# Kernel tuning notes

Measured on AMD Instinct MI355X. Metric: run time of the kernel, lower is better.

## Reference

```python
import jax, jax.numpy as jnp
import numpy as np

N = 20000      # total residues (nodes)
E = 320000     # contact edges
G = 16         # graphs in batch
D_IN = 1280    # ESM embedding dim
H = 256        # hidden channels (1=2=3)
C = 500        # GO classes
EPS = 1e-5


def setup_inputs() -> dict:
    key = jax.random.key(0)
    ks = jax.random.split(key, 16)
    s = 0.02
    return {
        "x": jax.random.normal(ks[0], (N, D_IN), jnp.float32),
        "edge_index": jax.random.randint(ks[1], (2, E), 0, N, jnp.int32),
        "edge_attr": jax.random.uniform(ks[2], (E, 1), jnp.float32),
        "batch": jnp.sort(jax.random.randint(ks[3], (N,), 0, G, jnp.int32)),
        "seq_emb": jax.random.normal(ks[4], (G, D_IN), jnp.float32),
        "W1": jax.random.normal(ks[5], (D_IN, H), jnp.float32) * s,
        "b1": jnp.zeros((H,), jnp.float32),
        "g1": jnp.ones((H,), jnp.float32),
        "be1": jnp.zeros((H,), jnp.float32),
        "W2": jax.random.normal(ks[6], (H, H), jnp.float32) * s,
        "b2": jnp.zeros((H,), jnp.float32),
        "g2": jnp.ones((H,), jnp.float32),
        "be2": jnp.zeros((H,), jnp.float32),
        "W3": jax.random.normal(ks[7], (H, H), jnp.float32) * s,
        "b3": jnp.zeros((H,), jnp.float32),
        "g3": jnp.ones((H,), jnp.float32),
        "be3": jnp.zeros((H,), jnp.float32),
        "fc1_w": jax.random.normal(ks[8], (D_IN, H), jnp.float32) * s,
        "fc1_b": jnp.zeros((H,), jnp.float32),
        "lin_w": jax.random.normal(ks[9], (H, C), jnp.float32) * s,
        "lin_b": jnp.zeros((C,), jnp.float32),
    }


def gcn_conv(x, row, col, ew, W, b):
    # PyG GCNConv: x' = D^{-1/2} (A + I) D^{-1/2} X W + b, with edge weights,
    # self-loops of weight 1, aggregation at target (col).
    xw = x @ W                                             # [N, H]
    deg = jax.ops.segment_sum(ew, col, num_segments=N) + 1.0
    dinv = jax.lax.rsqrt(deg)                              # [N]
    norm = dinv[row] * ew * dinv[col]                      # [E]
    agg = jax.ops.segment_sum(norm[:, None] * xw[row], col, num_segments=N)
    agg = agg + (dinv * dinv)[:, None] * xw                # self-loop term
    return agg + b


def batch_norm(x, g, b):
    # training-mode BN over the node dimension (biased variance, as torch)
    m = jnp.mean(x, axis=0)
    v = jnp.var(x, axis=0)
    return (x - m) * jax.lax.rsqrt(v + EPS) * g + b


def reference(x, edge_index, edge_attr, batch, seq_emb,
              W1, b1, g1, be1, W2, b2, g2, be2, W3, b3, g3, be3,
              fc1_w, fc1_b, lin_w, lin_b):
    row, col = edge_index[0], edge_index[1]
    ew = edge_attr[:, 0]

    h = batch_norm(jax.nn.relu(gcn_conv(x, row, col, ew, W1, b1)), g1, be1)
    h = batch_norm(jax.nn.relu(gcn_conv(h, row, col, ew, W2, b2)), g2, be2)
    h = batch_norm(gcn_conv(h, row, col, ew, W3, b3), g3, be3)

    # global_mean_pool over graphs
    sums = jax.ops.segment_sum(h, batch, num_segments=G)        # [G, H]
    cnt = jax.ops.segment_sum(jnp.ones((h.shape[0],), h.dtype), batch, num_segments=G)
    pooled = sums / jnp.maximum(cnt, 1.0)[:, None]

    y = seq_emb @ fc1_w + fc1_b                                 # [G, H]
    out = pooled + y
    # dropout skipped (eval mode)
    out = out @ lin_w + lin_b                                   # [G, C]
    return jax.nn.sigmoid(out)
```

## Files before the change

### kernel.cpp

```cpp
#include <hip/hip_runtime.h>
#include <hip/hip_bf16.h>
#include <math.h>

#define Nn 20000
#define En 320000
#define Gn 16
#define DINn 1280
#define Hn 256
#define Cn 500
#define EPSn 1e-5f
#define BNB 1024
#define SCB 256
#define SNB ((Nn + SCB - 1) / SCB)

typedef __attribute__((ext_vector_type(8))) short bf16x8;
typedef __attribute__((ext_vector_type(4))) float f32x4;

__device__ __forceinline__ float b2f(ushort u) {
    return __uint_as_float(((unsigned int)u) << 16);
}
__device__ __forceinline__ ushort f2b(float f) {
    __hip_bfloat16 h = __float2bfloat16(f);
    return *reinterpret_cast<ushort*>(&h);
}

#define GLOAD16(g, l) __builtin_amdgcn_global_load_lds( \
    (const __attribute__((address_space(1))) unsigned int*)(g), \
    (__attribute__((address_space(3))) unsigned int*)(l), 16, 0, 0)


__global__ void k_degcnt(const int* col, const float* ew, float* deg, int* counts) {
    int e = blockIdx.x * blockDim.x + threadIdx.x;
    if (e < En) {
        int c = col[e];
        atomicAdd(&deg[c], ew[e]);
        atomicAdd(&counts[c], 1);
    }
}

__global__ void k_dinv(const float* deg, float* dinv, float* dinv2) {
    int i = blockIdx.x * blockDim.x + threadIdx.x;
    if (i < Nn) {
        float d = deg[i] + 1.0f;
        float r = rsqrtf(d);
        dinv[i] = r;
        dinv2[i] = 1.0f / d;
    }
}


__global__ __launch_bounds__(SCB) void k_scanA(const int* __restrict__ counts,
                                               int* __restrict__ excl,
                                               int* __restrict__ blocksum) {
    __shared__ int sd[SCB];
    int t = threadIdx.x, b = blockIdx.x;
    int i = b * SCB + t;
    int v = (i < Nn) ? counts[i] : 0;
    sd[t] = v;
    __syncthreads();
    #pragma unroll
    for (int o = 1; o < SCB; o <<= 1) {
        int tv = (t >= o) ? sd[t - o] : 0;
        __syncthreads();
        sd[t] += tv;
        __syncthreads();
    }
    if (i < Nn) excl[i] = sd[t] - v;
    if (t == SCB - 1) blocksum[b] = sd[t];
}

__global__ __launch_bounds__(128) void k_scanB(const int* __restrict__ blocksum,
                                               int* __restrict__ blockoff,
                                               int* __restrict__ offsets) {
    __shared__ int sd[128];
    int t = threadIdx.x;
    int v = (t < SNB) ? blocksum[t] : 0;
    sd[t] = v;
    __syncthreads();
    #pragma unroll
    for (int o = 1; o < 128; o <<= 1) {
        int tv = (t >= o) ? sd[t - o] : 0;
        __syncthreads();
        sd[t] += tv;
        __syncthreads();
    }
    if (t < SNB) blockoff[t] = sd[t] - v;
    if (t == SNB - 1) offsets[Nn] = sd[t];
}

__global__ __launch_bounds__(SCB) void k_scanC(const int* __restrict__ excl,
                                               const int* __restrict__ blockoff,
                                               int* __restrict__ offsets,
                                               int* __restrict__ cursor) {
    int b = blockIdx.x;
    int i = b * SCB + threadIdx.x;
    if (i < Nn) {
        int o = excl[i] + blockoff[b];
        offsets[i] = o;
        cursor[i] = o;
    }
}

__global__ void k_fill2(const int* row, const int* col, const float* ew,
                        const float* dinv, int* cursor,
                        int* csr_row, float* csr_w) {
    int e = blockIdx.x * blockDim.x + threadIdx.x;
    if (e < En) {
        int r = row[e], c = col[e];
        int p = atomicAdd(&cursor[c], 1);
        csr_row[p] = r;
        csr_w[p] = dinv[r] * ew[e] * dinv[c];
    }
}


__global__ void k_gbounds(const int* __restrict__ batch, int* __restrict__ gstart) {
    int i = blockIdx.x * blockDim.x + threadIdx.x;
    if (i >= Nn) return;
    int b = batch[i];
    if (i == 0) {
        for (int g = 0; g <= b; g++) gstart[g] = 0;
    } else {
        int pb = batch[i - 1];
        for (int g = pb + 1; g <= b; g++) gstart[g] = i;
    }
    if (i == Nn - 1) {
        for (int g = b + 1; g <= Gn; g++) gstart[g] = Nn;
    }
}


__global__ __launch_bounds__(256) void k_x2bf(const float* __restrict__ x,
                                              ushort* __restrict__ xb) {
    size_t i = ((size_t)blockIdx.x * blockDim.x + threadIdx.x) * 8;
    const float4* xp = reinterpret_cast<const float4*>(&x[i]);
    float4 a = xp[0], b = xp[1];
    ushort t[8];
    t[0] = f2b(a.x); t[1] = f2b(a.y); t[2] = f2b(a.z); t[3] = f2b(a.w);
    t[4] = f2b(b.x); t[5] = f2b(b.y); t[6] = f2b(b.z); t[7] = f2b(b.w);
    *reinterpret_cast<uint4*>(&xb[i]) = *reinterpret_cast<uint4*>(&t[0]);
}


__global__ __launch_bounds__(256) void k_wt(const float* __restrict__ W,
                                            ushort* __restrict__ WT, int K) {
    __shared__ float tile[32][33];
    int k0 = blockIdx.x * 32, n0 = blockIdx.y * 32;
    int tx = threadIdx.x, ty = threadIdx.y;
    #pragma unroll
    for (int i = 0; i < 32; i += 8)
        tile[ty + i][tx] = W[(size_t)(k0 + ty + i) * Hn + n0 + tx];
    __syncthreads();
    #pragma unroll
    for (int i = 0; i < 32; i += 8)
        WT[(size_t)(n0 + ty + i) * K + k0 + tx] = f2b(tile[tx][ty + i]);
}


__global__ __launch_bounds__(256) void k_wtb(const float* __restrict__ W,
                                             const float* __restrict__ scaleA,
                                             const float* __restrict__ shiftA,
                                             ushort* __restrict__ WT,
                                             float* __restrict__ bv) {
    __shared__ float tile[32][33];
    int k0 = blockIdx.x * 32, n0 = blockIdx.y * 32;
    int tx = threadIdx.x, ty = threadIdx.y;
    #pragma unroll
    for (int i = 0; i < 32; i += 8)
        tile[ty + i][tx] = W[(size_t)(k0 + ty + i) * Hn + n0 + tx];
    __syncthreads();
    float sc = scaleA[k0 + tx], sh = shiftA[k0 + tx];
    #pragma unroll
    for (int i = 0; i < 32; i += 8) {
        float w = tile[tx][ty + i];
        WT[(size_t)(n0 + ty + i) * Hn + k0 + tx] = f2b(w * sc);
        float pb = w * sh;
        #pragma unroll
        for (int o = 16; o > 0; o >>= 1) pb += __shfl_down(pb, o, 32);
        if (tx == 0) atomicAdd(&bv[n0 + ty + i], pb);
    }
}


#define GBM 64
#define GBN 128
#define GBK 64

__global__ __launch_bounds__(256) void k_gemm_bf(
    const ushort* __restrict__ A, const ushort* __restrict__ BT,
    ushort* __restrict__ C, int M, int K, int NBL)
{
    __shared__ ushort Asl[2][GBM][GBK];
    __shared__ ushort Bsl[2][GBN][GBK];
    const int id = blockIdx.x;
    const int k8 = id >> 3;
    const int r8 = id & 7;
    const int p = (k8 >> 1) * 8 + r8;
    const int bnk = k8 & 1;
    if (p >= NBL) return;
    const int bm = p * GBM;
    const int bn = bnk * GBN;
    const int tid = threadIdx.x;
    const int lane = tid & 63;
    const int wid = tid >> 6;
    const int wm = wid >> 1, wn = wid & 1;
    const int l15 = lane & 15, l16 = lane >> 4;

    const int lrow = lane >> 3;
    const int lcolb = 16 * ((lane & 7) ^ lrow);

    f32x4 acc[2][4] = {};
    const int nt = K / GBK;

    auto STAGE = [&](int buf, int t) {
        const int k0 = t * GBK;
        #pragma unroll
        for (int c = 0; c < 2; c++) {
            int chunk = wid * 2 + c;
            int grow = bm + chunk * 8 + lrow;
            if (grow >= M) grow = M - 1;
            const char* src = (const char*)&A[(size_t)grow * K + k0] + lcolb;
            GLOAD16(src, &Asl[buf][chunk * 8][0]);
        }
        #pragma unroll
        for (int c = 0; c < 4; c++) {
            int chunk = wid * 4 + c;
            int grow = bn + chunk * 8 + lrow;
            const char* src = (const char*)&BT[(size_t)grow * K + k0] + lcolb;
            GLOAD16(src, &Bsl[buf][chunk * 8][0]);
        }
    };

    STAGE(0, 0);
    __syncthreads();

    for (int t = 0; t < nt; t++) {
        const int cur = t & 1;
        if (t + 1 < nt) STAGE(cur ^ 1, t + 1);
        #pragma unroll
        for (int ks = 0; ks < 2; ks++) {
            bf16x8 afr[2], bfr[4];
            #pragma unroll
            for (int i = 0; i < 2; i++) {
                int r = wm * 32 + i * 16 + l15;
                int cb = (ks * 64 + l16 * 16) ^ ((r & 7) << 4);
                afr[i] = *reinterpret_cast<const bf16x8*>((const char*)&Asl[cur][r][0] + cb);
            }
            #pragma unroll
            for (int j = 0; j < 4; j++) {
                int r = wn * 64 + j * 16 + l15;
                int cb = (ks * 64 + l16 * 16) ^ ((r & 7) << 4);
                bfr[j] = *reinterpret_cast<const bf16x8*>((const char*)&Bsl[cur][r][0] + cb);
            }
            #pragma unroll
            for (int i = 0; i < 2; i++)
                #pragma unroll
                for (int j = 0; j < 4; j++)
                    acc[i][j] = __builtin_amdgcn_mfma_f32_16x16x32_bf16(afr[i], bfr[j], acc[i][j], 0, 0, 0);
        }
        __syncthreads();
    }

    #pragma unroll
    for (int i = 0; i < 2; i++) {
        #pragma unroll
        for (int r = 0; r < 4; r++) {
            int grow = bm + wm * 32 + i * 16 + l16 * 4 + r;
            if (grow < M) {
                #pragma unroll
                for (int j = 0; j < 4; j++)
                    C[(size_t)grow * Hn + bn + wn * 64 + j * 16 + l15] = f2b(acc[i][j][r]);
            }
        }
    }
}


__device__ __forceinline__ void agg_accum(float* acc, float w, const uint4& v) {
    unsigned int u;
    u = v.x; acc[0] += w * b2f((ushort)u); acc[1] += w * b2f((ushort)(u >> 16));
    u = v.y; acc[2] += w * b2f((ushort)u); acc[3] += w * b2f((ushort)(u >> 16));
    u = v.z; acc[4] += w * b2f((ushort)u); acc[5] += w * b2f((ushort)(u >> 16));
    u = v.w; acc[6] += w * b2f((ushort)u); acc[7] += w * b2f((ushort)(u >> 16));
}

__global__ __launch_bounds__(256) void k_agg(const ushort* __restrict__ xw,
                                             const int* __restrict__ offsets,
                                             const int* __restrict__ csr_row,
                                             const float* __restrict__ csr_w,
                                             const float* __restrict__ dinv2,
                                             const float* __restrict__ bias,
                                             const float* __restrict__ bv,
                                             ushort* __restrict__ outp, int do_relu) {
    int node = blockIdx.x * 8 + (threadIdx.x >> 5);
    int l32 = threadIdx.x & 31;
    int s = offsets[node], e = offsets[node + 1];
    const uint4* xw4 = reinterpret_cast<const uint4*>(xw);

    float acc[8] = {};
    float wsum = 0.f;
    int k = s;
    for (; k + 4 <= e; k += 4) {
        int r0 = csr_row[k],     r1 = csr_row[k + 1];
        int r2 = csr_row[k + 2], r3 = csr_row[k + 3];
        float w0 = csr_w[k],     w1 = csr_w[k + 1];
        float w2 = csr_w[k + 2], w3 = csr_w[k + 3];
        uint4 v0 = xw4[(size_t)r0 * 32 + l32];
        uint4 v1 = xw4[(size_t)r1 * 32 + l32];
        uint4 v2 = xw4[(size_t)r2 * 32 + l32];
        uint4 v3 = xw4[(size_t)r3 * 32 + l32];
        wsum += (w0 + w1) + (w2 + w3);
        agg_accum(acc, w0, v0);
        agg_accum(acc, w1, v1);
        agg_accum(acc, w2, v2);
        agg_accum(acc, w3, v3);
    }
    for (; k < e; k++) {
        int r = csr_row[k];
        float w = csr_w[k];
        uint4 v = xw4[(size_t)r * 32 + l32];
        wsum += w;
        agg_accum(acc, w, v);
    }
    float d2 = dinv2[node];
    wsum += d2;
    uint4 vs = xw4[(size_t)node * 32 + l32];
    agg_accum(acc, d2, vs);

    const float4* bp = reinterpret_cast<const float4*>(&bias[l32 * 8]);
    float4 bb0 = bp[0], bb1 = bp[1];
    acc[0] += bb0.x; acc[1] += bb0.y; acc[2] += bb0.z; acc[3] += bb0.w;
    acc[4] += bb1.x; acc[5] += bb1.y; acc[6] += bb1.z; acc[7] += bb1.w;
    if (bv) {
        const float4* vp = reinterpret_cast<const float4*>(&bv[l32 * 8]);
        float4 bv0 = vp[0], bv1 = vp[1];
        acc[0] += wsum * bv0.x; acc[1] += wsum * bv0.y;
        acc[2] += wsum * bv0.z; acc[3] += wsum * bv0.w;
        acc[4] += wsum * bv1.x; acc[5] += wsum * bv1.y;
        acc[6] += wsum * bv1.z; acc[7] += wsum * bv1.w;
    }
    if (do_relu) {
        #pragma unroll
        for (int q = 0; q < 8; q++) acc[q] = fmaxf(acc[q], 0.f);
    }
    uint4 o;
    o.x = (unsigned int)f2b(acc[0]) | ((unsigned int)f2b(acc[1]) << 16);
    o.y = (unsigned int)f2b(acc[2]) | ((unsigned int)f2b(acc[3]) << 16);
    o.z = (unsigned int)f2b(acc[4]) | ((unsigned int)f2b(acc[5]) << 16);
    o.w = (unsigned int)f2b(acc[6]) | ((unsigned int)f2b(acc[7]) << 16);
    reinterpret_cast<uint4*>(outp)[(size_t)node * 32 + l32] = o;
}


__global__ __launch_bounds__(256) void k_bnpart(const ushort* __restrict__ h,
                                                float* __restrict__ partial) {
    int f = threadIdx.x;
    int blk = blockIdx.x;
    float s = 0.0f, ss = 0.0f;
    for (int i = blk; i < Nn; i += BNB) {
        float v = b2f(h[(size_t)i * Hn + f]);
        s += v;
        ss += v * v;
    }
    partial[(size_t)blk * 512 + f] = s;
    partial[(size_t)blk * 512 + 256 + f] = ss;
}

__global__ __launch_bounds__(256) void k_bnred(const float* __restrict__ partial,
                                               float* __restrict__ p2) {
    int f = threadIdx.x;
    int b = blockIdx.x;
    int b0 = b * 64;
    float s = 0.0f, ss = 0.0f;
    for (int j = 0; j < 64; j++) {
        const float* p = &partial[(size_t)(b0 + j) * 512];
        s += p[f];
        ss += p[256 + f];
    }
    p2[b * 512 + f] = s;
    p2[b * 512 + 256 + f] = ss;
}

__global__ void k_bnfinal2(const float* __restrict__ p2, const float* g, const float* be,
                           float* scaleA, float* shiftA) {
    int f = threadIdx.x;
    float s = 0.f, ss = 0.f;
    #pragma unroll
    for (int j = 0; j < 16; j++) {
        s += p2[j * 512 + f];
        ss += p2[j * 512 + 256 + f];
    }
    float mean = s / (float)Nn;
    float var = ss / (float)Nn - mean * mean;
    float a = g[f] * rsqrtf(var + EPSn);
    scaleA[f] = a;
    shiftA[f] = be[f] - mean * a;
}


#define PCH 32

__global__ __launch_bounds__(256) void k_pool2(const ushort* __restrict__ h,
                                               const int* __restrict__ gstart,
                                               const float* __restrict__ scaleA,
                                               const float* __restrict__ shiftA,
                                               float* __restrict__ pooled) {
    int g = blockIdx.x;
    int chunk = blockIdx.y;
    int f = threadIdx.x;
    int s = gstart[g], e = gstart[g + 1];
    int len = e - s;
    if (len <= 0) return;
    int per = (len + PCH - 1) / PCH;
    int cs = s + chunk * per;
    int ce = cs + per; if (ce > e) ce = e;
    if (cs >= ce) return;
    float sc = scaleA[f], sh = shiftA[f];
    float acc = 0.0f;
    for (int i = cs; i < ce; i++)
        acc += b2f(h[(size_t)i * Hn + f]) * sc + sh;
    atomicAdd(&pooled[g * Hn + f], acc);
}


__global__ __launch_bounds__(256) void k_head1part(const float* __restrict__ seq_emb,
                                                   const float* __restrict__ fc1_w,
                                                   float* __restrict__ hpart) {
    int g = blockIdx.x;
    int kc = blockIdx.y;
    int j = threadIdx.x;
    const float* se = &seq_emb[(size_t)g * DINn + kc * 128];
    const float* w = &fc1_w[(size_t)kc * 128 * Hn + j];
    float acc = 0.0f;
    #pragma unroll 8
    for (int k = 0; k < 128; k++)
        acc += se[k] * w[(size_t)k * Hn];
    hpart[((size_t)g * 10 + kc) * Hn + j] = acc;
}

__global__ __launch_bounds__(256) void k_head2f(const float* __restrict__ hpart,
                                                const float* __restrict__ fc1_b,
                                                const float* __restrict__ pooled,
                                                const int* __restrict__ gstart,
                                                const float* __restrict__ lin_w,
                                                const float* __restrict__ lin_b,
                                                float* __restrict__ out) {
    __shared__ float pf[Hn];
    int g = blockIdx.x;
    int half = blockIdx.y;
    int j = threadIdx.x;
    float s = fc1_b[j];
    #pragma unroll
    for (int kc = 0; kc < 10; kc++)
        s += hpart[((size_t)g * 10 + kc) * Hn + j];
    float cntf = fmaxf((float)(gstart[g + 1] - gstart[g]), 1.0f);
    pf[j] = pooled[g * Hn + j] / cntf + s;
    __syncthreads();
    int c = half * 250 + j;
    if (j < 250) {
        float a2 = lin_b[c];
        #pragma unroll 8
        for (int k = 0; k < Hn; k++)
            a2 += pf[k] * lin_w[(size_t)k * Cn + c];
        out[g * Cn + c] = 1.0f / (1.0f + expf(-a2));
    }
}


extern "C" void kernel_launch(void* const* d_in, const int* in_sizes, int n_in,
                              void* d_out, int out_size, void* d_ws, size_t ws_size,
                              hipStream_t stream) {
    const float* x        = (const float*)d_in[0];
    const int*   eidx     = (const int*)d_in[1];
    const float* eattr    = (const float*)d_in[2];
    const int*   batch    = (const int*)d_in[3];
    const float* seq_emb  = (const float*)d_in[4];
    const float* W1 = (const float*)d_in[5];
    const float* b1 = (const float*)d_in[6];
    const float* g1 = (const float*)d_in[7];
    const float* be1 = (const float*)d_in[8];
    const float* W2 = (const float*)d_in[9];
    const float* b2 = (const float*)d_in[10];
    const float* g2 = (const float*)d_in[11];
    const float* be2 = (const float*)d_in[12];
    const float* W3 = (const float*)d_in[13];
    const float* b3 = (const float*)d_in[14];
    const float* g3 = (const float*)d_in[15];
    const float* be3 = (const float*)d_in[16];
    const float* fc1_w = (const float*)d_in[17];
    const float* fc1_b = (const float*)d_in[18];
    const float* lin_w = (const float*)d_in[19];
    const float* lin_b = (const float*)d_in[20];
    float* out = (float*)d_out;

    const int* row = eidx;
    const int* col = eidx + En;

    char* ws = (char*)d_ws;
    size_t off = 0;
    auto alloc = [&](size_t bytes) -> char* {
        char* p = ws + off;
        off += (bytes + 255) & ~(size_t)255;
        return p;
    };
    ushort* xb     = (ushort*)alloc((size_t)Nn * DINn * 2);
    ushort* xwb    = (ushort*)alloc((size_t)Nn * Hn * 2);
    ushort* hb     = (ushort*)alloc((size_t)Nn * Hn * 2);
    char*  zbase   = ws + off;
    float* deg     = (float*)alloc(Nn * 4);
    int*   counts  = (int*)alloc(Nn * 4);
    float* bvA     = (float*)alloc(Hn * 4);
    float* bvB     = (float*)alloc(Hn * 4);
    float* pooled  = (float*)alloc(Gn * Hn * 4);
    size_t zspan   = (size_t)((ws + off) - zbase);
    float* dinv    = (float*)alloc(Nn * 4);
    float* dinv2   = (float*)alloc(Nn * 4);
    int*   offsets = (int*)alloc((Nn + 1) * 4);
    int*   cursor  = (int*)alloc(Nn * 4);
    int*   excl    = (int*)alloc(Nn * 4);
    int*   blocksum= (int*)alloc(SNB * 4);
    int*   blockoff= (int*)alloc(SNB * 4);
    int*   csr_row = (int*)alloc(En * 4);
    float* csr_w   = (float*)alloc(En * 4);
    float* scaleA  = (float*)alloc(Hn * 4);
    float* shiftA  = (float*)alloc(Hn * 4);
    int*   gstart  = (int*)alloc((Gn + 1) * 4);
    float* partial = (float*)alloc((size_t)BNB * 512 * 4);
    float* p2      = (float*)alloc(16 * 512 * 4);
    float* hpart   = (float*)alloc((size_t)Gn * 10 * Hn * 4);
    ushort* W1T    = (ushort*)alloc((size_t)Hn * DINn * 2);
    ushort* W2T    = (ushort*)alloc((size_t)Hn * Hn * 2);
    ushort* W3T    = (ushort*)alloc((size_t)Hn * Hn * 2);

    const int TB = 256;
    const int EB = (En + TB - 1) / TB;
    const int NB = (Nn + TB - 1) / TB;

    hipMemsetAsync(zbase, 0, zspan, stream);
    k_degcnt<<<EB, TB, 0, stream>>>(col, eattr, deg, counts);
    k_dinv<<<NB, TB, 0, stream>>>(deg, dinv, dinv2);
    k_scanA<<<SNB, SCB, 0, stream>>>(counts, excl, blocksum);
    k_scanB<<<1, 128, 0, stream>>>(blocksum, blockoff, offsets);
    k_scanC<<<SNB, SCB, 0, stream>>>(excl, blockoff, offsets, cursor);
    k_fill2<<<EB, TB, 0, stream>>>(row, col, eattr, dinv, cursor, csr_row, csr_w);
    k_gbounds<<<NB, TB, 0, stream>>>(batch, gstart);
    k_x2bf<<<(Nn * DINn / 8) / 256, 256, 0, stream>>>(x, xb);
    k_wt<<<dim3(DINn / 32, Hn / 32), dim3(32, 8), 0, stream>>>(W1, W1T, DINn);

    const int NBL = (Nn + GBM - 1) / GBM;
    const int GGRID = ((NBL * 2 + 15) / 16) * 16;
    const int AGB = Nn / 8;

    k_gemm_bf<<<GGRID, 256, 0, stream>>>(xb, W1T, xwb, Nn, DINn, NBL);
    k_agg<<<AGB, 256, 0, stream>>>(xwb, offsets, csr_row, csr_w, dinv2, b1, nullptr, hb, 1);
    k_bnpart<<<BNB, Hn, 0, stream>>>(hb, partial);
    k_bnred<<<16, Hn, 0, stream>>>(partial, p2);
    k_bnfinal2<<<1, Hn, 0, stream>>>(p2, g1, be1, scaleA, shiftA);

    k_wtb<<<dim3(Hn / 32, Hn / 32), dim3(32, 8), 0, stream>>>(W2, scaleA, shiftA, W2T, bvA);
    k_gemm_bf<<<GGRID, 256, 0, stream>>>(hb, W2T, xwb, Nn, Hn, NBL);
    k_agg<<<AGB, 256, 0, stream>>>(xwb, offsets, csr_row, csr_w, dinv2, b2, bvA, hb, 1);
    k_bnpart<<<BNB, Hn, 0, stream>>>(hb, partial);
    k_bnred<<<16, Hn, 0, stream>>>(partial, p2);
    k_bnfinal2<<<1, Hn, 0, stream>>>(p2, g2, be2, scaleA, shiftA);

    k_wtb<<<dim3(Hn / 32, Hn / 32), dim3(32, 8), 0, stream>>>(W3, scaleA, shiftA, W3T, bvB);
    k_gemm_bf<<<GGRID, 256, 0, stream>>>(hb, W3T, xwb, Nn, Hn, NBL);
    k_agg<<<AGB, 256, 0, stream>>>(xwb, offsets, csr_row, csr_w, dinv2, b3, bvB, hb, 0);
    k_bnpart<<<BNB, Hn, 0, stream>>>(hb, partial);
    k_bnred<<<16, Hn, 0, stream>>>(partial, p2);
    k_bnfinal2<<<1, Hn, 0, stream>>>(p2, g3, be3, scaleA, shiftA);

    k_pool2<<<dim3(Gn, PCH), Hn, 0, stream>>>(hb, gstart, scaleA, shiftA, pooled);
    k_head1part<<<dim3(Gn, 10), Hn, 0, stream>>>(seq_emb, fc1_w, hpart);
    k_head2f<<<dim3(Gn, 2), Hn, 0, stream>>>(hpart, fc1_b, pooled, gstart, lin_w, lin_b, out);
}
```

Baseline: 287.1 us.

## Fuse BatchNorm partial statistics into aggregation kernel and dinv into scan

The aggregation kernel now computes per-wave sums and sums of squares of its fp32 outputs, combining the two nodes in each 64-lane wave with a shuffle, and writes them as partials. This removes the separate k_bnpart pass that re-read the bf16 hidden matrix after each layer. The reduction stage is reshaped to handle 10000 partials across 64 blocks. The k_dinv kernel is also folded into k_scanA to save a launch. The statistics are now taken on the fp32 values before bf16 rounding, and the partial buffer and its reduction traffic are larger.

```diff
diff --git a/kernel.cpp b/kernel.cpp
--- a/kernel.cpp
+++ b/kernel.cpp
@@ -9,9 +9,11 @@
 #define Hn 256
 #define Cn 500
 #define EPSn 1e-5f
-#define BNB 1024
 #define SCB 256
 #define SNB ((Nn + SCB - 1) / SCB)
+#define AGB (Nn / 8)
+#define NPART (AGB * 4)
+#define RB 64
 
 typedef __attribute__((ext_vector_type(8))) short bf16x8;
 typedef __attribute__((ext_vector_type(4))) float f32x4;
@@ -38,20 +40,13 @@
     }
 }
 
-__global__ void k_dinv(const float* deg, float* dinv, float* dinv2) {
-    int i = blockIdx.x * blockDim.x + threadIdx.x;
-    if (i < Nn) {
-        float d = deg[i] + 1.0f;
-        float r = rsqrtf(d);
-        dinv[i] = r;
-        dinv2[i] = 1.0f / d;
-    }
-}
-
 
 __global__ __launch_bounds__(SCB) void k_scanA(const int* __restrict__ counts,
+                                               const float* __restrict__ deg,
                                                int* __restrict__ excl,
-                                               int* __restrict__ blocksum) {
+                                               int* __restrict__ blocksum,
+                                               float* __restrict__ dinv,
+                                               float* __restrict__ dinv2) {
     __shared__ int sd[SCB];
     int t = threadIdx.x, b = blockIdx.x;
     int i = b * SCB + t;
@@ -65,7 +60,12 @@
         sd[t] += tv;
         __syncthreads();
     }
-    if (i < Nn) excl[i] = sd[t] - v;
+    if (i < Nn) {
+        excl[i] = sd[t] - v;
+        float d = deg[i] + 1.0f;
+        dinv[i] = rsqrtf(d);
+        dinv2[i] = 1.0f / d;
+    }
     if (t == SCB - 1) blocksum[b] = sd[t];
 }
 
@@ -291,7 +291,9 @@
                                              const float* __restrict__ dinv2,
                                              const float* __restrict__ bias,
                                              const float* __restrict__ bv,
-                                             ushort* __restrict__ outp, int do_relu) {
+                                             ushort* __restrict__ outp,
+                                             float* __restrict__ partial,
+                                             int do_relu) {
     int node = blockIdx.x * 8 + (threadIdx.x >> 5);
     int l32 = threadIdx.x & 31;
     int s = offsets[node], e = offsets[node + 1];
@@ -349,33 +351,38 @@
     o.z = (unsigned int)f2b(acc[4]) | ((unsigned int)f2b(acc[5]) << 16);
     o.w = (unsigned int)f2b(acc[6]) | ((unsigned int)f2b(acc[7]) << 16);
     reinterpret_cast<uint4*>(outp)[(size_t)node * 32 + l32] = o;
-}
-
-
-__global__ __launch_bounds__(256) void k_bnpart(const ushort* __restrict__ h,
-                                                float* __restrict__ partial) {
-    int f = threadIdx.x;
-    int blk = blockIdx.x;
-    float s = 0.0f, ss = 0.0f;
-    for (int i = blk; i < Nn; i += BNB) {
-        float v = b2f(h[(size_t)i * Hn + f]);
-        s += v;
-        ss += v * v;
-    }
-    partial[(size_t)blk * 512 + f] = s;
-    partial[(size_t)blk * 512 + 256 + f] = ss;
-}
+
+    float s8[8], q8[8];
+    #pragma unroll
+    for (int q = 0; q < 8; q++) {
+        float a = acc[q];
+        float aa = a * a;
+        s8[q] = a + __shfl_xor(a, 32);
+        q8[q] = aa + __shfl_xor(aa, 32);
+    }
+    if ((threadIdx.x & 63) < 32) {
+        int wv = threadIdx.x >> 6;
+        float* pr = &partial[((size_t)blockIdx.x * 4 + wv) * 512];
+        float4 a0 = {s8[0], s8[1], s8[2], s8[3]};
+        float4 a1 = {s8[4], s8[5], s8[6], s8[7]};
+        float4 b0 = {q8[0], q8[1], q8[2], q8[3]};
+        float4 b1 = {q8[4], q8[5], q8[6], q8[7]};
+        reinterpret_cast<float4*>(pr)[l32 * 2] = a0;
+        reinterpret_cast<float4*>(pr)[l32 * 2 + 1] = a1;
+        reinterpret_cast<float4*>(pr + 256)[l32 * 2] = b0;
+        reinterpret_cast<float4*>(pr + 256)[l32 * 2 + 1] = b1;
+    }
+}
+
 
 __global__ __launch_bounds__(256) void k_bnred(const float* __restrict__ partial,
                                                float* __restrict__ p2) {
     int f = threadIdx.x;
     int b = blockIdx.x;
-    int b0 = b * 64;
     float s = 0.0f, ss = 0.0f;
-    for (int j = 0; j < 64; j++) {
-        const float* p = &partial[(size_t)(b0 + j) * 512];
-        s += p[f];
-        ss += p[256 + f];
+    for (int j = b; j < NPART; j += RB) {
+        s += partial[(size_t)j * 512 + f];
+        ss += partial[(size_t)j * 512 + 256 + f];
     }
     p2[b * 512 + f] = s;
     p2[b * 512 + 256 + f] = ss;
@@ -386,7 +393,7 @@
     int f = threadIdx.x;
     float s = 0.f, ss = 0.f;
     #pragma unroll
-    for (int j = 0; j < 16; j++) {
+    for (int j = 0; j < RB; j++) {
         s += p2[j * 512 + f];
         ss += p2[j * 512 + 256 + f];
     }
@@ -525,8 +532,8 @@
     float* scaleA  = (float*)alloc(Hn * 4);
     float* shiftA  = (float*)alloc(Hn * 4);
     int*   gstart  = (int*)alloc((Gn + 1) * 4);
-    float* partial = (float*)alloc((size_t)BNB * 512 * 4);
-    float* p2      = (float*)alloc(16 * 512 * 4);
+    float* partial = (float*)alloc((size_t)NPART * 512 * 4);
+    float* p2      = (float*)alloc(RB * 512 * 4);
     float* hpart   = (float*)alloc((size_t)Gn * 10 * Hn * 4);
     ushort* W1T    = (ushort*)alloc((size_t)Hn * DINn * 2);
     ushort* W2T    = (ushort*)alloc((size_t)Hn * Hn * 2);
@@ -538,8 +545,7 @@
 
     hipMemsetAsync(zbase, 0, zspan, stream);
     k_degcnt<<<EB, TB, 0, stream>>>(col, eattr, deg, counts);
-    k_dinv<<<NB, TB, 0, stream>>>(deg, dinv, dinv2);
-    k_scanA<<<SNB, SCB, 0, stream>>>(counts, excl, blocksum);
+    k_scanA<<<SNB, SCB, 0, stream>>>(counts, deg, excl, blocksum, dinv, dinv2);
     k_scanB<<<1, 128, 0, stream>>>(blocksum, blockoff, offsets);
     k_scanC<<<SNB, SCB, 0, stream>>>(excl, blockoff, offsets, cursor);
     k_fill2<<<EB, TB, 0, stream>>>(row, col, eattr, dinv, cursor, csr_row, csr_w);
@@ -549,26 +555,22 @@
 
     const int NBL = (Nn + GBM - 1) / GBM;
     const int GGRID = ((NBL * 2 + 15) / 16) * 16;
-    const int AGB = Nn / 8;
 
     k_gemm_bf<<<GGRID, 256, 0, stream>>>(xb, W1T, xwb, Nn, DINn, NBL);
-    k_agg<<<AGB, 256, 0, stream>>>(xwb, offsets, csr_row, csr_w, dinv2, b1, nullptr, hb, 1);
-    k_bnpart<<<BNB, Hn, 0, stream>>>(hb, partial);
-    k_bnred<<<16, Hn, 0, stream>>>(partial, p2);
+    k_agg<<<AGB, 256, 0, stream>>>(xwb, offsets, csr_row, csr_w, dinv2, b1, nullptr, hb, partial, 1);
+    k_bnred<<<RB, Hn, 0, stream>>>(partial, p2);
     k_bnfinal2<<<1, Hn, 0, stream>>>(p2, g1, be1, scaleA, shiftA);
 
     k_wtb<<<dim3(Hn / 32, Hn / 32), dim3(32, 8), 0, stream>>>(W2, scaleA, shiftA, W2T, bvA);
     k_gemm_bf<<<GGRID, 256, 0, stream>>>(hb, W2T, xwb, Nn, Hn, NBL);
-    k_agg<<<AGB, 256, 0, stream>>>(xwb, offsets, csr_row, csr_w, dinv2, b2, bvA, hb, 1);
-    k_bnpart<<<BNB, Hn, 0, stream>>>(hb, partial);
-    k_bnred<<<16, Hn, 0, stream>>>(partial, p2);
+    k_agg<<<AGB, 256, 0, stream>>>(xwb, offsets, csr_row, csr_w, dinv2, b2, bvA, hb, partial, 1);
+    k_bnred<<<RB, Hn, 0, stream>>>(partial, p2);
     k_bnfinal2<<<1, Hn, 0, stream>>>(p2, g2, be2, scaleA, shiftA);
 
     k_wtb<<<dim3(Hn / 32, Hn / 32), dim3(32, 8), 0, stream>>>(W3, scaleA, shiftA, W3T, bvB);
     k_gemm_bf<<<GGRID, 256, 0, stream>>>(hb, W3T, xwb, Nn, Hn, NBL);
-    k_agg<<<AGB, 256, 0, stream>>>(xwb, offsets, csr_row, csr_w, dinv2, b3, bvB, hb, 0);
-    k_bnpart<<<BNB, Hn, 0, stream>>>(hb, partial);
-    k_bnred<<<16, Hn, 0, stream>>>(partial, p2);
+    k_agg<<<AGB, 256, 0, stream>>>(xwb, offsets, csr_row, csr_w, dinv2, b3, bvB, hb, partial, 0);
+    k_bnred<<<RB, Hn, 0, stream>>>(partial, p2);
     k_bnfinal2<<<1, Hn, 0, stream>>>(p2, g3, be3, scaleA, shiftA);
 
     k_pool2<<<dim3(Gn, PCH), Hn, 0, stream>>>(hb, gstart, scaleA, shiftA, pooled);
```

After: 393.0 us. 36.9% more time.
